# Kernel optimization log

Hardware: AMD Instinct MI355X
Metric: run time of the kernel (lower is better)

Reference implementation:

```python
import jax, jax.numpy as jnp
import numpy as np

FEAT_DIM = 1024
NUM_HEAD = 8


def setup_inputs() -> dict:
    key = jax.random.key(0)
    ks = jax.random.split(key, 8)
    D = FEAT_DIM
    s = D ** -0.5
    return {
        "motion": jax.random.normal(ks[0], (8, 1024, D), dtype=jnp.float32),
        "scene_feats": jax.random.normal(ks[1], (8, 2048, D), dtype=jnp.float32),
        # nn.Linear weights stored as [in, out] (already transposed for x @ W)
        "Wq": jax.random.normal(ks[2], (D, D), dtype=jnp.float32) * s,
        "bq": jax.random.normal(ks[3], (D,), dtype=jnp.float32) * s,
        "Wkv": jax.random.normal(ks[4], (D, 2 * D), dtype=jnp.float32) * s,
        "bkv": jax.random.normal(ks[5], (2 * D,), dtype=jnp.float32) * s,
        "Wout": jax.random.normal(ks[6], (D, D), dtype=jnp.float32) * s,
        "bout": jax.random.normal(ks[7], (D,), dtype=jnp.float32) * s,
    }


def reference(motion, scene_feats, Wq, bq, Wkv, bkv, Wout, bout):
    bs, L, D = motion.shape
    N = scene_feats.shape[1]
    H = NUM_HEAD
    Dh = D // H

    # q scaled by full feat_dim**-0.5 (as in source, not head_dim)
    q = (motion @ Wq + bq) * (D ** -0.5)
    kv = scene_feats @ Wkv + bkv
    k, v = kv[..., :D], kv[..., D:]

    # Faithful to source: q is viewed as (bs, H, L, Dh) with NO transpose,
    # while k, v use view(bs, N, H, Dh) followed by transpose(1, 2).
    q = q.reshape(bs, H, L, Dh)                      # [bs,H,L,Dh] (layout quirk)
    k = k.reshape(bs, N, H, Dh).transpose(0, 2, 1, 3)  # [bs,H,N,Dh]
    v = v.reshape(bs, N, H, Dh).transpose(0, 2, 1, 3)  # [bs,H,N,Dh]

    att = jnp.einsum("bhld,bhnd->bhln", q, k)        # [bs,H,L,N]
    att = jax.nn.softmax(att, axis=-1)
    out = jnp.einsum("bhln,bhnd->bhld", att, v)      # [bs,H,L,Dh]
    out = out.reshape(bs, L, D)                      # contiguous view, matches torch .view
    return out @ Wout + bout
```

## Files before the change

### kernel.cpp

```cpp
#include <hip/hip_runtime.h>

typedef __attribute__((ext_vector_type(8))) short bf16x8;
typedef __attribute__((ext_vector_type(4))) float f32x4;
typedef __attribute__((ext_vector_type(4))) unsigned int u32x4;
typedef __attribute__((ext_vector_type(4))) float f32x4v;

#define MFMA16(a,b,c) __builtin_amdgcn_mfma_f32_16x16x32_bf16((a),(b),(c),0,0,0)

__device__ __forceinline__ short f2bf(float f){
  unsigned u = __builtin_bit_cast(unsigned, f);
  u += 0x7fffu + ((u >> 16) & 1u);
  return (short)(u >> 16);
}

__device__ __forceinline__ void gload16(const void* g, void* l){
  __builtin_amdgcn_global_load_lds((const __attribute__((address_space(1))) unsigned*)g,
                                   (__attribute__((address_space(3))) unsigned*)l,
                                   16, 0, 0);
}

__global__ __launch_bounds__(256) void k_f2bf(const float* __restrict__ in,
                                              short* __restrict__ out, int n8){
  int i = blockIdx.x * 256 + threadIdx.x;
  if (i >= n8) return;
  f32x4v a = ((const f32x4v*)in)[i*2];
  f32x4v b = ((const f32x4v*)in)[i*2+1];
  bf16x8 o;
  o[0]=f2bf(a[0]); o[1]=f2bf(a[1]); o[2]=f2bf(a[2]); o[3]=f2bf(a[3]);
  o[4]=f2bf(b[0]); o[5]=f2bf(b[1]); o[6]=f2bf(b[2]); o[7]=f2bf(b[3]);
  ((bf16x8*)out)[i] = o;
}

__global__ __launch_bounds__(256) void k_prep_wT(const float* __restrict__ W,
                                                 short* __restrict__ Wt, int K, int N){
  int i = blockIdx.x * 256 + threadIdx.x;
  int total = (K >> 3) * N;
  if (i >= total) return;
  int n  = i % N;
  int k0 = (i / N) << 3;
  bf16x8 o;
#pragma unroll
  for (int j = 0; j < 8; ++j) o[j] = f2bf(W[(size_t)(k0 + j) * N + n]);
  *(bf16x8*)&Wt[(size_t)n * K + k0] = o;
}

__global__ __launch_bounds__(256) void k_transpose_v(const short* __restrict__ V,
                                                     short* __restrict__ Vt){
  int bh = blockIdx.y;
  int n0 = blockIdx.x * 64;
  int tid = threadIdx.x;
  int n = n0 + (tid & 63);
  int dhg = (tid >> 6) * 8;
  const short* vbase = V  + (size_t)bh * 2048 * 128;
  short*       tbase = Vt + (size_t)bh * 128 * 2048;
#pragma unroll
  for (int p = 0; p < 4; ++p){
    int dh0 = p * 32 + dhg;
    bf16x8 v = *(const bf16x8*)&vbase[(size_t)n * 128 + dh0];
#pragma unroll
    for (int j = 0; j < 8; ++j)
      tbase[(size_t)(dh0 + j) * 2048 + n] = v[j];
  }
}

template<int MODE>
__global__ __launch_bounds__(256, 2) void k_gemm(
    const short* __restrict__ A, const short* __restrict__ Bt,
    const float* __restrict__ bias, float scale,
    void* __restrict__ out0, void* __restrict__ out1,
    int M, int N, int K)
{
  __shared__ __align__(16) short Alds[2][128 * 32];
  __shared__ __align__(16) short Blds[2][128 * 32];
  const int tid = threadIdx.x;
  const int l = tid & 63, w = tid >> 6;
  const int m0 = blockIdx.y * 128, n0 = blockIdx.x * 128;
  const int wr = w >> 1, wc = w & 1;
  const int lr = l & 15, lg = l >> 4;

  const int srow = l >> 2;
  const int scol = 8 * ((l & 3) ^ (srow & 3));
  const int acol = 8 * (lg ^ (lr & 3));

  f32x4 acc[4][4];
#pragma unroll
  for (int a = 0; a < 4; ++a)
#pragma unroll
    for (int b = 0; b < 4; ++b) acc[a][b] = (f32x4)(0.0f);

  const int nk = K >> 5;
  auto stage = [&](int kt, int buf){
    int k0 = kt << 5;
#pragma unroll
    for (int i = 0; i < 4; ++i){
      int c = w * 4 + i;
      if (c < 8){
        int m = c * 16 + srow;
        gload16(A + (size_t)(m0 + m) * K + k0 + scol, &Alds[buf][c * 512]);
      } else {
        int n = (c - 8) * 16 + srow;
        gload16(Bt + (size_t)(n0 + n) * K + k0 + scol, &Blds[buf][(c - 8) * 512]);
      }
    }
  };

  stage(0, 0);
  __syncthreads();
  int cur = 0;
  for (int kt = 0; kt < nk; ++kt){
    if (kt + 1 < nk) stage(kt + 1, cur ^ 1);
    bf16x8 af[4], bfv[4];
#pragma unroll
    for (int mi = 0; mi < 4; ++mi){
      int row = wr * 64 + mi * 16 + lr;
      af[mi] = *(const bf16x8*)&Alds[cur][row * 32 + acol];
    }
#pragma unroll
    for (int ni = 0; ni < 4; ++ni){
      int row = wc * 64 + ni * 16 + lr;
      bfv[ni] = *(const bf16x8*)&Blds[cur][row * 32 + acol];
    }
#pragma unroll
    for (int mi = 0; mi < 4; ++mi)
#pragma unroll
      for (int ni = 0; ni < 4; ++ni)
        acc[mi][ni] = MFMA16(af[mi], bfv[ni], acc[mi][ni]);
    __syncthreads();
    cur ^= 1;
  }

#pragma unroll
  for (int mi = 0; mi < 4; ++mi)
#pragma unroll
    for (int ni = 0; ni < 4; ++ni){
      int col = n0 + wc * 64 + ni * 16 + lr;
      float bv = bias[col];
#pragma unroll
      for (int r = 0; r < 4; ++r){
        int row = m0 + wr * 64 + mi * 16 + lg * 4 + r;
        float v = acc[mi][ni][r] + bv;
        if (MODE == 0){
          v *= scale;
          int b = row >> 10, lp = row & 1023;
          int h = lp >> 7;
          int lq = ((lp & 127) << 3) | (col >> 7);
          int dh = col & 127;
          ((short*)out0)[(((size_t)(b * 8 + h)) * 1024 + lq) * 128 + dh] = f2bf(v);
        } else if (MODE == 1){
          int b = row >> 11, nn = row & 2047;
          if (col < 1024){
            int h = col >> 7, dh = col & 127;
            ((short*)out0)[(((size_t)(b * 8 + h)) * 2048 + nn) * 128 + dh] = f2bf(v);
          } else {
            int c2 = col - 1024, h = c2 >> 7, dh = c2 & 127;
            ((short*)out1)[(((size_t)(b * 8 + h)) * 2048 + nn) * 128 + dh] = f2bf(v);
          }
        } else {
          ((float*)out0)[(size_t)row * N + col] = v;
        }
      }
    }
}

__global__ __launch_bounds__(256, 2) void k_attn(
    const short* __restrict__ Q, const short* __restrict__ K,
    const short* __restrict__ Vt, short* __restrict__ O)
{
  __shared__ __align__(16) short Klds[64][136];
  __shared__ __align__(16) short Vlds[128][72];
  __shared__ __align__(16) short Plds[4][16][72];
  const int tid = threadIdx.x;
  const int l = tid & 63, w = tid >> 6;
  const int bh = blockIdx.y;
  const int q0 = blockIdx.x * 64;
  const int lr = l & 15, lg = l >> 4;

  const short* Qb = Q  + (size_t)bh * 1024 * 128;
  const short* Kb = K  + (size_t)bh * 2048 * 128;
  const short* Vb = Vt + (size_t)bh * 128 * 2048;

  const int qrow = q0 + w * 16 + lr;
  bf16x8 qf[4];
#pragma unroll
  for (int kc = 0; kc < 4; ++kc)
    qf[kc] = *(const bf16x8*)&Qb[(size_t)qrow * 128 + kc * 32 + lg * 8];

  f32x4 acc[8];
#pragma unroll
  for (int d = 0; d < 8; ++d) acc[d] = (f32x4)(0.0f);
  float mrun[4], lrun[4];
#pragma unroll
  for (int r = 0; r < 4; ++r){ mrun[r] = -3e38f; lrun[r] = 0.f; }

  u32x4 kreg[4], vreg[4];
  auto loadregs = [&](int t){
    int kv0 = t * 64;
#pragma unroll
    for (int p = 0; p < 4; ++p){
      kreg[p] = *(const u32x4*)&Kb[(size_t)(kv0 + p * 16 + (tid >> 4)) * 128 + (tid & 15) * 8];
      vreg[p] = *(const u32x4*)&Vb[(size_t)(p * 32 + (tid >> 3)) * 2048 + kv0 + (tid & 7) * 8];
    }
  };
  auto writelds = [&](){
#pragma unroll
    for (int p = 0; p < 4; ++p){
      *(u32x4*)&Klds[p * 16 + (tid >> 4)][(tid & 15) * 8] = kreg[p];
      *(u32x4*)&Vlds[p * 32 + (tid >> 3)][(tid & 7) * 8] = vreg[p];
    }
  };

  loadregs(0);
  for (int t = 0; t < 32; ++t){
    __syncthreads();
    writelds();
    __syncthreads();
    if (t + 1 < 32) loadregs(t + 1);

    f32x4 s[4];
#pragma unroll
    for (int nt = 0; nt < 4; ++nt){
      f32x4 sv = (f32x4)(0.0f);
#pragma unroll
      for (int kc = 0; kc < 4; ++kc){
        bf16x8 kf = *(const bf16x8*)&Klds[nt * 16 + lr][kc * 32 + lg * 8];
        sv = MFMA16(qf[kc], kf, sv);
      }
      s[nt] = sv;
    }

    float mnew[4], sc[4], rsum[4];
#pragma unroll
    for (int r = 0; r < 4; ++r){
      float v = fmaxf(fmaxf(s[0][r], s[1][r]), fmaxf(s[2][r], s[3][r]));
      v = fmaxf(v, __shfl_xor(v, 1, 16));
      v = fmaxf(v, __shfl_xor(v, 2, 16));
      v = fmaxf(v, __shfl_xor(v, 4, 16));
      v = fmaxf(v, __shfl_xor(v, 8, 16));
      mnew[r] = fmaxf(mrun[r], v);
      sc[r] = exp2f(mrun[r] - mnew[r]);
      mrun[r] = mnew[r];
      rsum[r] = 0.f;
    }
#pragma unroll
    for (int nt = 0; nt < 4; ++nt)
#pragma unroll
      for (int r = 0; r < 4; ++r){
        float p = exp2f(s[nt][r] - mnew[r]);
        rsum[r] += p;
        Plds[w][lg * 4 + r][nt * 16 + lr] = f2bf(p);
      }
#pragma unroll
    for (int r = 0; r < 4; ++r){
      float rs = rsum[r];
      rs += __shfl_xor(rs, 1, 16);
      rs += __shfl_xor(rs, 2, 16);
      rs += __shfl_xor(rs, 4, 16);
      rs += __shfl_xor(rs, 8, 16);
      lrun[r] = lrun[r] * sc[r] + rs;
#pragma unroll
      for (int d = 0; d < 8; ++d) acc[d][r] *= sc[r];
    }

    bf16x8 pa[2];
#pragma unroll
    for (int kc = 0; kc < 2; ++kc)
      pa[kc] = *(const bf16x8*)&Plds[w][lr][kc * 32 + lg * 8];
#pragma unroll
    for (int d = 0; d < 8; ++d)
#pragma unroll
      for (int kc = 0; kc < 2; ++kc){
        bf16x8 vf = *(const bf16x8*)&Vlds[d * 16 + lr][kc * 32 + lg * 8];
        acc[d] = MFMA16(pa[kc], vf, acc[d]);
      }
  }

  const int b = bh >> 3, h = bh & 7;
#pragma unroll
  for (int r = 0; r < 4; ++r){
    float inv = 1.0f / lrun[r];
    int grow = q0 + w * 16 + lg * 4 + r;
    size_t base = ((size_t)b * 1024 + (size_t)h * 128 + (grow >> 3)) * 1024
                + (size_t)(grow & 7) * 128;
#pragma unroll
    for (int d = 0; d < 8; ++d)
      O[base + d * 16 + lr] = f2bf(acc[d][r] * inv);
  }
}

extern "C" void kernel_launch(void* const* d_in, const int* in_sizes, int n_in,
                              void* d_out, int out_size, void* d_ws, size_t ws_size,
                              hipStream_t stream){
  const float* motion = (const float*)d_in[0];
  const float* scene  = (const float*)d_in[1];
  const float* Wq     = (const float*)d_in[2];
  const float* bq     = (const float*)d_in[3];
  const float* Wkv    = (const float*)d_in[4];
  const float* bkv    = (const float*)d_in[5];
  const float* Wout   = (const float*)d_in[6];
  const float* bout   = (const float*)d_in[7];
  float* out = (float*)d_out;

  char* ws = (char*)d_ws;
  const size_t MB = 1024 * 1024;
  short* WqT   = (short*)(ws + 0);
  short* WkvT  = (short*)(ws + 2  * MB);
  short* WoutT = (short*)(ws + 6  * MB);
  short* mA    = (short*)(ws + 8  * MB);
  short* sA    = (short*)(ws + 24 * MB);
  short* Qb    = (short*)(ws + 56 * MB);
  short* Kb    = (short*)(ws + 72 * MB);
  short* Vb    = (short*)(ws + 104* MB);
  short* attnO = mA;
  short* Vtb   = sA;

  const float qscale = 0.03125f * 1.44269504088896341f;

  k_prep_wT<<<dim3(512),  256, 0, stream>>>(Wq,   WqT,   1024, 1024);
  k_prep_wT<<<dim3(1024), 256, 0, stream>>>(Wkv,  WkvT,  1024, 2048);
  k_prep_wT<<<dim3(512),  256, 0, stream>>>(Wout, WoutT, 1024, 1024);
  k_f2bf<<<dim3(4096), 256, 0, stream>>>(motion, mA, 1024 * 1024);
  k_f2bf<<<dim3(8192), 256, 0, stream>>>(scene,  sA, 2 * 1024 * 1024);

  k_gemm<0><<<dim3(8, 64),   256, 0, stream>>>(mA, WqT,  bq,  qscale, Qb, nullptr, 8192, 1024, 1024);
  k_gemm<1><<<dim3(16, 128), 256, 0, stream>>>(sA, WkvT, bkv, 1.0f,   Kb, Vb,     16384, 2048, 1024);
  k_transpose_v<<<dim3(32, 64), 256, 0, stream>>>(Vb, Vtb);
  k_attn<<<dim3(16, 64), 256, 0, stream>>>(Qb, Kb, Vtb, attnO);
  k_gemm<2><<<dim3(8, 64), 256, 0, stream>>>(attnO, WoutT, bout, 1.0f, out, nullptr, 8192, 1024, 1024);
}
```

Baseline: 355.9 us.

## Rework attention kernel with async LDS staging, larger tiles, lazy rescale, fused V transpose

Removes the separate V transpose kernel by having the KV GEMM write V directly in transposed layout. The attention kernel now uses double-buffered direct global-to-LDS loads with XOR swizzling instead of register staging with two barriers per step. Each wave also processes 32 query rows instead of 16, so every K/V fragment read is reused twice. Softmax rescaling is skipped unless a row max grows by more than a threshold, and blocks are remapped so heads group by XCD. The costs are more registers, larger LDS use that may limit occupancy, and scattered strided stores in the GEMM epilogue.

After: 345.1 us. 1.03x faster.

```diff
diff --git a/kernel.cpp b/kernel.cpp
--- a/kernel.cpp
+++ b/kernel.cpp
@@ -2,7 +2,6 @@
 
 typedef __attribute__((ext_vector_type(8))) short bf16x8;
 typedef __attribute__((ext_vector_type(4))) float f32x4;
-typedef __attribute__((ext_vector_type(4))) unsigned int u32x4;
 typedef __attribute__((ext_vector_type(4))) float f32x4v;
 
 #define MFMA16(a,b,c) __builtin_amdgcn_mfma_f32_16x16x32_bf16((a),(b),(c),0,0,0)
@@ -42,25 +41,6 @@
 #pragma unroll
   for (int j = 0; j < 8; ++j) o[j] = f2bf(W[(size_t)(k0 + j) * N + n]);
   *(bf16x8*)&Wt[(size_t)n * K + k0] = o;
-}
-
-__global__ __launch_bounds__(256) void k_transpose_v(const short* __restrict__ V,
-                                                     short* __restrict__ Vt){
-  int bh = blockIdx.y;
-  int n0 = blockIdx.x * 64;
-  int tid = threadIdx.x;
-  int n = n0 + (tid & 63);
-  int dhg = (tid >> 6) * 8;
-  const short* vbase = V  + (size_t)bh * 2048 * 128;
-  short*       tbase = Vt + (size_t)bh * 128 * 2048;
-#pragma unroll
-  for (int p = 0; p < 4; ++p){
-    int dh0 = p * 32 + dhg;
-    bf16x8 v = *(const bf16x8*)&vbase[(size_t)n * 128 + dh0];
-#pragma unroll
-    for (int j = 0; j < 8; ++j)
-      tbase[(size_t)(dh0 + j) * 2048 + n] = v[j];
-  }
 }
 
 template<int MODE>
@@ -153,7 +133,7 @@
             ((short*)out0)[(((size_t)(b * 8 + h)) * 2048 + nn) * 128 + dh] = f2bf(v);
           } else {
             int c2 = col - 1024, h = c2 >> 7, dh = c2 & 127;
-            ((short*)out1)[(((size_t)(b * 8 + h)) * 2048 + nn) * 128 + dh] = f2bf(v);
+            ((short*)out1)[(((size_t)(b * 8 + h)) * 128 + dh) * 2048 + nn] = f2bf(v);
           }
         } else {
           ((float*)out0)[(size_t)row * N + col] = v;
@@ -166,125 +146,165 @@
     const short* __restrict__ Q, const short* __restrict__ K,
     const short* __restrict__ Vt, short* __restrict__ O)
 {
-  __shared__ __align__(16) short Klds[64][136];
-  __shared__ __align__(16) short Vlds[128][72];
-  __shared__ __align__(16) short Plds[4][16][72];
+  __shared__ __align__(16) short Klds[2][64 * 128];
+  __shared__ __align__(16) short Vlds[2][128 * 64];
+  __shared__ __align__(16) short Plds[4][32 * 64];
   const int tid = threadIdx.x;
   const int l = tid & 63, w = tid >> 6;
-  const int bh = blockIdx.y;
-  const int q0 = blockIdx.x * 64;
   const int lr = l & 15, lg = l >> 4;
+
+  int flat = blockIdx.y * 8 + blockIdx.x;
+  int xcd = flat & 7, idx = flat >> 3;
+  int bh = xcd * 8 + (idx >> 3);
+  int q0 = (idx & 7) * 128;
 
   const short* Qb = Q  + (size_t)bh * 1024 * 128;
   const short* Kb = K  + (size_t)bh * 2048 * 128;
   const short* Vb = Vt + (size_t)bh * 128 * 2048;
 
-  const int qrow = q0 + w * 16 + lr;
-  bf16x8 qf[4];
-#pragma unroll
-  for (int kc = 0; kc < 4; ++kc)
-    qf[kc] = *(const bf16x8*)&Qb[(size_t)qrow * 128 + kc * 32 + lg * 8];
-
-  f32x4 acc[8];
-#pragma unroll
-  for (int d = 0; d < 8; ++d) acc[d] = (f32x4)(0.0f);
-  float mrun[4], lrun[4];
-#pragma unroll
-  for (int r = 0; r < 4; ++r){ mrun[r] = -3e38f; lrun[r] = 0.f; }
-
-  u32x4 kreg[4], vreg[4];
-  auto loadregs = [&](int t){
+  bf16x8 qf[2][4];
+#pragma unroll
+  for (int mi = 0; mi < 2; ++mi)
+#pragma unroll
+    for (int kc = 0; kc < 4; ++kc)
+      qf[mi][kc] = *(const bf16x8*)&Qb[(size_t)(q0 + w * 32 + mi * 16 + lr) * 128 + kc * 32 + lg * 8];
+
+  f32x4 acc[8][2];
+#pragma unroll
+  for (int d = 0; d < 8; ++d){ acc[d][0] = (f32x4)(0.0f); acc[d][1] = (f32x4)(0.0f); }
+  float mrun[2][4], lsum[2][4];
+#pragma unroll
+  for (int mi = 0; mi < 2; ++mi)
+#pragma unroll
+    for (int r = 0; r < 4; ++r){ mrun[mi][r] = -3e38f; lsum[mi][r] = 0.f; }
+
+  auto stageK = [&](int t, int buf){
     int kv0 = t * 64;
 #pragma unroll
-    for (int p = 0; p < 4; ++p){
-      kreg[p] = *(const u32x4*)&Kb[(size_t)(kv0 + p * 16 + (tid >> 4)) * 128 + (tid & 15) * 8];
-      vreg[p] = *(const u32x4*)&Vb[(size_t)(p * 32 + (tid >> 3)) * 2048 + kv0 + (tid & 7) * 8];
+    for (int i = 0; i < 4; ++i){
+      int c = w * 4 + i;
+      int row = 4 * c + (l >> 4);
+      int col = ((l & 15) * 8) ^ ((row & 7) * 8);
+      gload16(Kb + (size_t)(kv0 + row) * 128 + col, &Klds[buf][c * 512]);
     }
   };
-  auto writelds = [&](){
-#pragma unroll
-    for (int p = 0; p < 4; ++p){
-      *(u32x4*)&Klds[p * 16 + (tid >> 4)][(tid & 15) * 8] = kreg[p];
-      *(u32x4*)&Vlds[p * 32 + (tid >> 3)][(tid & 7) * 8] = vreg[p];
+  auto stageV = [&](int t, int buf){
+    int kv0 = t * 64;
+#pragma unroll
+    for (int i = 0; i < 4; ++i){
+      int c = w * 4 + i;
+      int dh = 8 * c + (l >> 3);
+      int col = ((l & 7) * 8) ^ (((l >> 3) & 7) * 8);
+      gload16(Vb + (size_t)dh * 2048 + kv0 + col, &Vlds[buf][c * 512]);
     }
   };
 
-  loadregs(0);
+  stageK(0, 0); stageV(0, 0);
+  __syncthreads();
+  int cur = 0;
+  const int swz = (lr & 7) * 8;
+
   for (int t = 0; t < 32; ++t){
+    if (t + 1 < 32){ stageK(t + 1, cur ^ 1); stageV(t + 1, cur ^ 1); }
+    const short* Kl = &Klds[cur][0];
+    const short* Vl = &Vlds[cur][0];
+    short* Pw = &Plds[w][0];
+
+    f32x4 s[2][4];
+#pragma unroll
+    for (int nt = 0; nt < 4; ++nt){
+      f32x4 s0 = (f32x4)(0.0f), s1 = (f32x4)(0.0f);
+#pragma unroll
+      for (int kc = 0; kc < 4; ++kc){
+        bf16x8 kf = *(const bf16x8*)&Kl[(nt * 16 + lr) * 128 + ((kc * 32 + lg * 8) ^ swz)];
+        s0 = MFMA16(qf[0][kc], kf, s0);
+        s1 = MFMA16(qf[1][kc], kf, s1);
+      }
+      s[0][nt] = s0; s[1][nt] = s1;
+    }
+
+    float pmax[2][4];
+    int ok = 1;
+#pragma unroll
+    for (int mi = 0; mi < 2; ++mi)
+#pragma unroll
+      for (int r = 0; r < 4; ++r){
+        float v = fmaxf(fmaxf(s[mi][0][r], s[mi][1][r]), fmaxf(s[mi][2][r], s[mi][3][r]));
+        pmax[mi][r] = v;
+        ok &= (v <= mrun[mi][r] + 8.0f) ? 1 : 0;
+      }
+    if (!__all(ok)){
+#pragma unroll
+      for (int mi = 0; mi < 2; ++mi)
+#pragma unroll
+        for (int r = 0; r < 4; ++r){
+          float v = pmax[mi][r];
+          v = fmaxf(v, __shfl_xor(v, 1, 16));
+          v = fmaxf(v, __shfl_xor(v, 2, 16));
+          v = fmaxf(v, __shfl_xor(v, 4, 16));
+          v = fmaxf(v, __shfl_xor(v, 8, 16));
+          float mnew = fmaxf(mrun[mi][r], v);
+          float sc = exp2f(mrun[mi][r] - mnew);
+          mrun[mi][r] = mnew;
+          lsum[mi][r] *= sc;
+#pragma unroll
+          for (int d = 0; d < 8; ++d) acc[d][mi][r] *= sc;
+        }
+    }
+
+#pragma unroll
+    for (int mi = 0; mi < 2; ++mi)
+#pragma unroll
+      for (int r = 0; r < 4; ++r){
+        int row = mi * 16 + lg * 4 + r;
+        int rsw = (row & 7) * 8;
+        float ls = 0.f;
+#pragma unroll
+        for (int nt = 0; nt < 4; ++nt){
+          float p = exp2f(s[mi][nt][r] - mrun[mi][r]);
+          ls += p;
+          Pw[row * 64 + ((nt * 16 + lr) ^ rsw)] = f2bf(p);
+        }
+        lsum[mi][r] += ls;
+      }
+
+    bf16x8 pa[2][2];
+#pragma unroll
+    for (int mi = 0; mi < 2; ++mi)
+#pragma unroll
+      for (int kc = 0; kc < 2; ++kc)
+        pa[mi][kc] = *(const bf16x8*)&Pw[(mi * 16 + lr) * 64 + ((kc * 32 + lg * 8) ^ swz)];
+#pragma unroll
+    for (int d = 0; d < 8; ++d)
+#pragma unroll
+      for (int kc = 0; kc < 2; ++kc){
+        bf16x8 vf = *(const bf16x8*)&Vl[(d * 16 + lr) * 64 + ((kc * 32 + lg * 8) ^ swz)];
+        acc[d][0] = MFMA16(pa[0][kc], vf, acc[d][0]);
+        acc[d][1] = MFMA16(pa[1][kc], vf, acc[d][1]);
+      }
+
     __syncthreads();
-    writelds();
-    __syncthreads();
-    if (t + 1 < 32) loadregs(t + 1);
-
-    f32x4 s[4];
-#pragma unroll
-    for (int nt = 0; nt < 4; ++nt){
-      f32x4 sv = (f32x4)(0.0f);
-#pragma unroll
-      for (int kc = 0; kc < 4; ++kc){
-        bf16x8 kf = *(const bf16x8*)&Klds[nt * 16 + lr][kc * 32 + lg * 8];
-        sv = MFMA16(qf[kc], kf, sv);
-      }
-      s[nt] = sv;
-    }
-
-    float mnew[4], sc[4], rsum[4];
+    cur ^= 1;
+  }
+
+  const int b = bh >> 3, h = bh & 7;
+#pragma unroll
+  for (int mi = 0; mi < 2; ++mi)
 #pragma unroll
     for (int r = 0; r < 4; ++r){
-      float v = fmaxf(fmaxf(s[0][r], s[1][r]), fmaxf(s[2][r], s[3][r]));
-      v = fmaxf(v, __shfl_xor(v, 1, 16));
-      v = fmaxf(v, __shfl_xor(v, 2, 16));
-      v = fmaxf(v, __shfl_xor(v, 4, 16));
-      v = fmaxf(v, __shfl_xor(v, 8, 16));
-      mnew[r] = fmaxf(mrun[r], v);
-      sc[r] = exp2f(mrun[r] - mnew[r]);
-      mrun[r] = mnew[r];
-      rsum[r] = 0.f;
-    }
-#pragma unroll
-    for (int nt = 0; nt < 4; ++nt)
-#pragma unroll
-      for (int r = 0; r < 4; ++r){
-        float p = exp2f(s[nt][r] - mnew[r]);
-        rsum[r] += p;
-        Plds[w][lg * 4 + r][nt * 16 + lr] = f2bf(p);
-      }
-#pragma unroll
-    for (int r = 0; r < 4; ++r){
-      float rs = rsum[r];
-      rs += __shfl_xor(rs, 1, 16);
-      rs += __shfl_xor(rs, 2, 16);
-      rs += __shfl_xor(rs, 4, 16);
-      rs += __shfl_xor(rs, 8, 16);
-      lrun[r] = lrun[r] * sc[r] + rs;
-#pragma unroll
-      for (int d = 0; d < 8; ++d) acc[d][r] *= sc[r];
-    }
-
-    bf16x8 pa[2];
-#pragma unroll
-    for (int kc = 0; kc < 2; ++kc)
-      pa[kc] = *(const bf16x8*)&Plds[w][lr][kc * 32 + lg * 8];
-#pragma unroll
-    for (int d = 0; d < 8; ++d)
-#pragma unroll
-      for (int kc = 0; kc < 2; ++kc){
-        bf16x8 vf = *(const bf16x8*)&Vlds[d * 16 + lr][kc * 32 + lg * 8];
-        acc[d] = MFMA16(pa[kc], vf, acc[d]);
-      }
-  }
-
-  const int b = bh >> 3, h = bh & 7;
-#pragma unroll
-  for (int r = 0; r < 4; ++r){
-    float inv = 1.0f / lrun[r];
-    int grow = q0 + w * 16 + lg * 4 + r;
-    size_t base = ((size_t)b * 1024 + (size_t)h * 128 + (grow >> 3)) * 1024
-                + (size_t)(grow & 7) * 128;
-#pragma unroll
-    for (int d = 0; d < 8; ++d)
-      O[base + d * 16 + lr] = f2bf(acc[d][r] * inv);
-  }
+      float ls = lsum[mi][r];
+      ls += __shfl_xor(ls, 1, 16);
+      ls += __shfl_xor(ls, 2, 16);
+      ls += __shfl_xor(ls, 4, 16);
+      ls += __shfl_xor(ls, 8, 16);
+      float inv = 1.0f / ls;
+      int grow = q0 + w * 32 + mi * 16 + lg * 4 + r;
+      size_t base = ((size_t)b * 1024 + (size_t)h * 128 + (grow >> 3)) * 1024
+                  + (size_t)(grow & 7) * 128;
+#pragma unroll
+      for (int d = 0; d < 8; ++d)
+        O[base + d * 16 + lr] = f2bf(acc[d][mi][r] * inv);
+    }
 }
 
 extern "C" void kernel_launch(void* const* d_in, const int* in_sizes, int n_in,
@@ -309,9 +329,8 @@
   short* sA    = (short*)(ws + 24 * MB);
   short* Qb    = (short*)(ws + 56 * MB);
   short* Kb    = (short*)(ws + 72 * MB);
-  short* Vb    = (short*)(ws + 104* MB);
+  short* Vtb   = (short*)(ws + 104* MB);
   short* attnO = mA;
-  short* Vtb   = sA;
 
   const float qscale = 0.03125f * 1.44269504088896341f;
 
@@ -322,8 +341,7 @@
   k_f2bf<<<dim3(8192), 256, 0, stream>>>(scene,  sA, 2 * 1024 * 1024);
 
   k_gemm<0><<<dim3(8, 64),   256, 0, stream>>>(mA, WqT,  bq,  qscale, Qb, nullptr, 8192, 1024, 1024);
-  k_gemm<1><<<dim3(16, 128), 256, 0, stream>>>(sA, WkvT, bkv, 1.0f,   Kb, Vb,     16384, 2048, 1024);
-  k_transpose_v<<<dim3(32, 64), 256, 0, stream>>>(Vb, Vtb);
-  k_attn<<<dim3(16, 64), 256, 0, stream>>>(Qb, Kb, Vtb, attnO);
+  k_gemm<1><<<dim3(16, 128), 256, 0, stream>>>(sA, WkvT, bkv, 1.0f,   Kb, Vtb,    16384, 2048, 1024);
+  k_attn<<<dim3(8, 64), 256, 0, stream>>>(Qb, Kb, Vtb, attnO);
   k_gemm<2><<<dim3(8, 64), 256, 0, stream>>>(attnO, WoutT, bout, 1.0f, out, nullptr, 8192, 1024, 1024);
 }
```
